# Kernel optimization log

Hardware: AMD Instinct MI355X
Metric: run time of the kernel (lower is better)

The kernel has to match this reference:

```python
import jax, jax.numpy as jnp
import numpy as np

INNER_DIM = 64
NEG = -1e12


def _rope_rotate(x, cos_pos, sin_pos):
    # x: [b, s, d]; rotate interleaved pairs as in the torch code
    x2 = jnp.stack([-x[..., 1::2], x[..., 0::2]], axis=-1).reshape(x.shape)
    return x * cos_pos + x2 * sin_pos


def setup_inputs() -> dict:
    key = jax.random.key(0)
    ks = jax.random.split(key, 5)
    b, s, h, f = 8, 1024, 768, 32
    hid = h + f  # 800
    inner, t = INNER_DIM, 9
    return {
        "last_hidden_state": jax.random.normal(ks[0], (b, s, h), jnp.float32),
        "hand_features": jax.random.normal(ks[1], (b, s, f), jnp.float32),
        "attention_mask": jnp.ones((b, s), jnp.int32),
        "W1": jax.random.normal(ks[2], (hid, 2 * inner), jnp.float32) * 0.02,
        "b1": jnp.zeros((2 * inner,), jnp.float32),
        "W2": jax.random.normal(ks[3], (hid, 2 * t), jnp.float32) * 0.02,
        "b2": jnp.zeros((2 * t,), jnp.float32),
    }


def reference(last_hidden_state, hand_features, attention_mask, W1, b1, W2, b2):
    h = jnp.concatenate([last_hidden_state, hand_features], axis=-1)  # [b,s,800]
    out = h @ W1 + b1                                                  # [b,s,2*inner]
    qw, kw = out[..., 0::2], out[..., 1::2]                            # [b,s,inner]

    s = h.shape[1]
    d = qw.shape[-1]
    # SinusoidalPositionEmbedding 'zero': interleaved sin (even) / cos (odd)
    pos = jnp.arange(s, dtype=jnp.float32)
    freqs = jnp.power(10000.0, -2.0 * jnp.arange(d // 2, dtype=jnp.float32) / d)
    ang = pos[:, None] * freqs[None, :]          # [s, d/2]
    cos_pos = jnp.repeat(jnp.cos(ang), 2, axis=-1)  # [s, d]
    sin_pos = jnp.repeat(jnp.sin(ang), 2, axis=-1)

    qw = _rope_rotate(qw, cos_pos, sin_pos)
    kw = _rope_rotate(kw, cos_pos, sin_pos)

    logits = jnp.einsum('bmd,bnd->bmn', qw, kw) / (d ** 0.5)           # [b,s,s]

    bias = jnp.einsum('bnh->bhn', h @ W2 + b2) / 2.0                   # [b,2t,s]
    logits = logits[:, None] + bias[:, 0::2, None, :] + bias[:, 1::2, :, None]  # [b,t,s,s]

    # sequence masking on both trailing axes
    m = attention_mask.astype(logits.dtype)                            # [b,s]
    mq = m[:, None, :, None]  # mask over axis -2 (rows)
    mk = m[:, None, None, :]  # mask over axis -1 (cols)
    logits = logits * mq + NEG * (1.0 - mq)
    logits = logits * mk + NEG * (1.0 - mk)

    # strictly-lower-triangular penalty (row > col)
    idx = jnp.arange(s)
    tril = (idx[:, None] > idx[None, :]).astype(logits.dtype)          # [s,s]
    logits = logits - tril * (-NEG)
    return logits
```

## Files before the change

### kernel.cpp

```cpp
#include <hip/hip_runtime.h>
#include <math.h>

#define B_   8
#define S_   1024
#define HDIM 768
#define FDIM 32
#define KDIM 800
#define D_   64
#define KSTEPS 25

constexpr float NEGV = -1000000000000.0f;

typedef __attribute__((ext_vector_type(8))) short short8;
typedef __attribute__((ext_vector_type(4))) float f32x4;

static __device__ __forceinline__ unsigned short f2bf(float f) {
    unsigned int x = __float_as_uint(f);
    unsigned int r = (x + 0x7fffu + ((x >> 16) & 1u)) >> 16;
    return (unsigned short)r;
}
static __device__ __forceinline__ unsigned int pack2(float a, float b) {
    return (unsigned int)f2bf(a) | ((unsigned int)f2bf(b) << 16);
}

union frag_cast { unsigned int u[4]; short8 s8; };

__global__ __launch_bounds__(256) void k0_prep(
    const float* __restrict__ W1, const float* __restrict__ b1,
    const float* __restrict__ W2, const float* __restrict__ b2,
    unsigned short* __restrict__ Wt, float* __restrict__ bv,
    float2* __restrict__ rope)
{
    const int tid = threadIdx.x;
    if (blockIdx.x >= 25) {
        int e = (blockIdx.x - 25) * 256 + tid;
#pragma unroll
        for (int t = 0; t < 16; ++t, e += 2048) {
            const int s = e >> 5, i = e & 31;
            const float freq = exp2f(-(float)i * 0.4152410119f);
            float sv, cv;
            sincosf((float)s * freq, &sv, &cv);
            rope[e] = make_float2(cv, sv);
        }
        return;
    }

    __shared__ float shW[32][136];
    __shared__ float shW2[32][20];
    const int k0 = blockIdx.x << 5;
#pragma unroll
    for (int p = 0; p < 4; ++p) {
        const int flat = tid + (p << 8);
        const int kk = flat >> 5;
        const int c4 = (flat & 31) << 2;
        const float4 v = *(const float4*)(W1 + (size_t)(k0 + kk) * 128 + c4);
        shW[kk][c4 + 0] = v.x; shW[kk][c4 + 1] = v.y;
        shW[kk][c4 + 2] = v.z; shW[kk][c4 + 3] = v.w;
    }
    for (int i = tid; i < 576; i += 256)
        shW2[i / 18][i % 18] = W2[(size_t)k0 * 18 + i];
    __syncthreads();

    for (int i = tid; i < 768; i += 256) {
        const int tile = i >> 6, g = (i >> 4) & 3, col = i & 15;
        const int nc = tile * 16 + col;
        unsigned int pk[4];
#pragma unroll
        for (int h = 0; h < 4; ++h) {
            const int ka = g * 8 + 2 * h, kb = ka + 1;
            float a, b;
            if (nc < 64)       { a = shW[ka][2*nc];          b = shW[kb][2*nc]; }
            else if (nc < 128) { a = shW[ka][2*(nc-64)+1];   b = shW[kb][2*(nc-64)+1]; }
            else if (nc < 146) { a = shW2[ka][nc-128];       b = shW2[kb][nc-128]; }
            else               { a = 0.0f; b = 0.0f; }
            pk[h] = pack2(a, b);
        }
        *(uint4*)(Wt + ((size_t)blockIdx.x * 768 + i) * 8) =
            make_uint4(pk[0], pk[1], pk[2], pk[3]);
    }
    if (blockIdx.x == 0 && tid < 192) {
        float v = tid < 64  ? b1[2 * tid]
                : tid < 128 ? b1[2 * (tid - 64) + 1]
                : tid < 146 ? b2[tid - 128] : 0.0f;
        bv[tid] = v;
    }
}

__global__ __launch_bounds__(256) void k1_proj(
    const float* __restrict__ lhs, const float* __restrict__ hf,
    const unsigned short* __restrict__ Wt, const float* __restrict__ bv,
    const float2* __restrict__ rope,
    unsigned short* __restrict__ qw, unsigned short* __restrict__ kw,
    float* __restrict__ bias_t)
{
    __shared__ __align__(16) unsigned short repack[16][128];

    const int tid  = threadIdx.x;
    const int m0   = blockIdx.x << 4;
    const int lane = tid & 63;
    const int w    = tid >> 6;
    const int r16  = lane & 15;
    const int g    = lane >> 4;

    const float* arow = lhs + (size_t)(m0 + r16) * HDIM;
    const float* hrow = hf  + (size_t)(m0 + r16) * FDIM;
    const unsigned short* wbase = Wt + ((size_t)(w * 3 * 64 + (g << 4) + r16)) * 8;

    float4 ab[4][2];
    uint4  bb[4][3];

    auto loadA = [&](int c, float4* dst) {
        const int k = (c << 5) + (g << 3);
        const float* src = (k < HDIM) ? (arow + k) : (hrow + (k - HDIM));
        dst[0] = *(const float4*)src;
        dst[1] = *(const float4*)(src + 4);
    };
    auto loadB = [&](int c, uint4* dst) {
        const unsigned short* p = wbase + (size_t)c * 768 * 8;
#pragma unroll
        for (int u = 0; u < 3; ++u)
            dst[u] = *(const uint4*)(p + u * 64 * 8);
    };

    f32x4 acc[3];
    const f32x4 zero = {0.0f, 0.0f, 0.0f, 0.0f};
#pragma unroll
    for (int u = 0; u < 3; ++u) acc[u] = zero;

    auto consume = [&](const float4* aA, const uint4* bB) {
        frag_cast fa;
        fa.u[0] = pack2(aA[0].x, aA[0].y);
        fa.u[1] = pack2(aA[0].z, aA[0].w);
        fa.u[2] = pack2(aA[1].x, aA[1].y);
        fa.u[3] = pack2(aA[1].z, aA[1].w);
#pragma unroll
        for (int u = 0; u < 3; ++u) {
            frag_cast fb;
            fb.u[0] = bB[u].x; fb.u[1] = bB[u].y;
            fb.u[2] = bB[u].z; fb.u[3] = bB[u].w;
            acc[u] = __builtin_amdgcn_mfma_f32_16x16x32_bf16(fa.s8, fb.s8, acc[u], 0, 0, 0);
        }
    };

#pragma unroll
    for (int d = 0; d < 4; ++d) { loadA(d, ab[d]); loadB(d, bb[d]); }

#pragma unroll
    for (int cb = 0; cb < 24; cb += 4) {
#pragma unroll
        for (int d = 0; d < 4; ++d) {
            const int c = cb + d;
            consume(ab[d], bb[d]);
            if (c + 4 < KSTEPS) { loadA(c + 4, ab[d]); loadB(c + 4, bb[d]); }
        }
    }
    consume(ab[0], bb[0]);

    const int bidx = m0 >> 10;
    const int s0   = m0 & (S_ - 1);
#pragma unroll
    for (int u = 0; u < 3; ++u) {
        const int tile = w * 3 + u;
        if (tile < 8) {
            const int jj  = (tile < 4 ? tile : tile - 4) * 16 + r16;
            const int fi  = jj >> 1;
            const float bvv = bv[tile * 16 + r16];
            const float sgn = (jj & 1) ? 1.0f : -1.0f;
            const float scl = (tile < 4) ? 0.125f : 1.0f;
            float x[4], p[4];
#pragma unroll
            for (int rr = 0; rr < 4; ++rr) x[rr] = acc[u][rr] + bvv;
#pragma unroll
            for (int rr = 0; rr < 4; ++rr) p[rr] = __shfl_xor(x[rr], 1, 64);
            const int cbase = (tile < 4 ? 0 : 64) + jj;
#pragma unroll
            for (int rr = 0; rr < 4; ++rr) {
                const float2 cs = rope[((s0 + g * 4 + rr) << 5) + fi];
                repack[g * 4 + rr][cbase] =
                    f2bf(fmaf(p[rr], sgn * cs.y, x[rr] * cs.x) * scl);
            }
        } else if (tile < 10) {
            const int cc = (tile - 8) * 16 + r16;
            if (cc < 18) {
                const float bvv = bv[tile * 16 + r16];
                f32x4 v;
#pragma unroll
                for (int rr = 0; rr < 4; ++rr) v[rr] = (acc[u][rr] + bvv) * 0.5f;
                *(f32x4*)(bias_t + (((size_t)(bidx * 18 + cc)) << 10) + s0 + g * 4) = v;
            }
        }
    }
    __syncthreads();
    {
        const int row = tid >> 4, seg = tid & 15;
        const uint4 v = *(const uint4*)&repack[row][seg * 8];
        if (seg < 8) *(uint4*)(qw + ((size_t)(m0 + row)) * D_ + seg * 8) = v;
        else         *(uint4*)(kw + ((size_t)(m0 + row)) * D_ + (seg - 8) * 8) = v;
    }
}

__global__ __launch_bounds__(256) void k2_logits(
    const unsigned short* __restrict__ qw, const unsigned short* __restrict__ kw,
    const float* __restrict__ bias_t, const int* __restrict__ mask,
    float* __restrict__ out)
{
    __shared__ __align__(16) char smem_u[64 * 66 * 4];
    __shared__ float bn[18][64];
    __shared__ float bm[18][64];
    __shared__ float mqf[64], mkf[64];
    unsigned short* qsm = (unsigned short*)smem_u;
    unsigned short* ksm = qsm + 64 * 64;
    float* tbuf = (float*)smem_u;

    const int tid = threadIdx.x;
    int bid;
    {
        const int i = blockIdx.x;
        bid = (i & 7) * 256 + (i >> 3);
    }
    const int b   = bid >> 8;
    const int rem = bid & 255;
    const int m0  = (rem >> 4) << 6;
    const int n0  = (rem & 15) << 6;

#pragma unroll
    for (int u = 0; u < 2; ++u) {
        const int idx = tid + (u << 8);
        const int row = idx >> 3;
        const int c8  = idx & 7;
        const int sb  = (row << 7) + ((c8 ^ (row & 7)) << 4);
        const uint4 vq = *(const uint4*)(qw + ((size_t)(b << 10) + m0 + row) * D_ + (c8 << 3));
        *(uint4*)((char*)qsm + sb) = vq;
        const uint4 vk = *(const uint4*)(kw + ((size_t)(b << 10) + n0 + row) * D_ + (c8 << 3));
        *(uint4*)((char*)ksm + sb) = vk;
    }
    for (int idx = tid; idx < 18 * 64; idx += 256) {
        const int c = idx >> 6;
        const int x = idx & 63;
        bn[c][x] = bias_t[(((size_t)(b * 18 + c)) << 10) + n0 + x];
        bm[c][x] = bias_t[(((size_t)(b * 18 + c)) << 10) + m0 + x];
    }
    if (tid < 64)        mqf[tid]      = (float)mask[b * S_ + m0 + tid];
    else if (tid < 128)  mkf[tid - 64] = (float)mask[b * S_ + n0 + (tid - 64)];
    __syncthreads();

    const int lane = tid & 63;
    const int w    = tid >> 6;
    const int wr   = w >> 1;
    const int wc   = w & 1;
    const int r16  = lane & 15;
    const int g    = lane >> 4;

    f32x4 acc[2][2];
    const f32x4 zero = {0.0f, 0.0f, 0.0f, 0.0f};
#pragma unroll
    for (int mi = 0; mi < 2; ++mi)
#pragma unroll
        for (int ni = 0; ni < 2; ++ni) acc[mi][ni] = zero;

#pragma unroll
    for (int ku = 0; ku < 2; ++ku) {
        short8 af[2], bf[2];
#pragma unroll
        for (int mi = 0; mi < 2; ++mi) {
            const int row  = wr * 32 + mi * 16 + r16;
            const int slot = ((ku << 2) + g) ^ (row & 7);
            af[mi] = *(const short8*)((const char*)qsm + (row << 7) + (slot << 4));
        }
#pragma unroll
        for (int ni = 0; ni < 2; ++ni) {
            const int row  = wc * 32 + ni * 16 + r16;
            const int slot = ((ku << 2) + g) ^ (row & 7);
            bf[ni] = *(const short8*)((const char*)ksm + (row << 7) + (slot << 4));
        }
#pragma unroll
        for (int mi = 0; mi < 2; ++mi)
#pragma unroll
            for (int ni = 0; ni < 2; ++ni)
                acc[mi][ni] = __builtin_amdgcn_mfma_f32_16x16x32_bf16(
                    af[mi], bf[ni], acc[mi][ni], 0, 0, 0);
    }

    __syncthreads();
#pragma unroll
    for (int mi = 0; mi < 2; ++mi)
#pragma unroll
        for (int ni = 0; ni < 2; ++ni)
#pragma unroll
            for (int rr = 0; rr < 4; ++rr)
                tbuf[(wr * 32 + mi * 16 + g * 4 + rr) * 66 +
                     wc * 32 + ni * 16 + r16] = acc[mi][ni][rr];
    __syncthreads();

    const int rb = tid >> 4;
    const int c4 = (tid & 15) << 2;
    const float fk0 = mkf[c4 + 0], fk1 = mkf[c4 + 1],
                fk2 = mkf[c4 + 2], fk3 = mkf[c4 + 3];

    float  p[4][4], accp[4][4];
    size_t base[4];
#pragma unroll
    for (int i = 0; i < 4; ++i) {
        const int row = rb + (i << 4);
        const int rg  = m0 + row;
        const float fm = mqf[row];
        const f32x4 a = *(const f32x4*)&tbuf[row * 66 + c4];
        const float fkk[4] = {fk0, fk1, fk2, fk3};
#pragma unroll
        for (int j = 0; j < 4; ++j) {
            const float fk = fkk[j];
            const float pj = fm * fk;
            float ad = NEGV * ((1.0f - fm) * fk + (1.0f - fk));
            if (rg > n0 + c4 + j) ad += NEGV;
            p[i][j]    = pj;
            accp[i][j] = fmaf(a[j], pj, ad);
        }
        base[i] = (((size_t)(b * 9)) << 20) + ((size_t)rg << 10) + n0 + c4;
    }

#pragma unroll
    for (int t = 0; t < 9; ++t) {
        const f32x4 bnv = *(const f32x4*)&bn[2 * t][c4];
        const size_t toff = (size_t)t << 20;
#pragma unroll
        for (int i = 0; i < 4; ++i) {
            const float bmv = bm[2 * t + 1][rb + (i << 4)];
            f32x4 v;
#pragma unroll
            for (int j = 0; j < 4; ++j)
                v[j] = fmaf(bnv[j] + bmv, p[i][j], accp[i][j]);
            *(f32x4*)(out + base[i] + toff) = v;
        }
    }
}

extern "C" void kernel_launch(void* const* d_in, const int* in_sizes, int n_in,
                              void* d_out, int out_size, void* d_ws, size_t ws_size,
                              hipStream_t stream) {
    const float* lhs  = (const float*)d_in[0];
    const float* hf   = (const float*)d_in[1];
    const int*   mask = (const int*)  d_in[2];
    const float* W1   = (const float*)d_in[3];
    const float* b1   = (const float*)d_in[4];
    const float* W2   = (const float*)d_in[5];
    const float* b2   = (const float*)d_in[6];
    float* out = (float*)d_out;

    unsigned short* qw = (unsigned short*)d_ws;
    unsigned short* kw = qw + (size_t)B_ * S_ * D_;
    float* bias_t = (float*)((char*)d_ws + (4u << 20));
    unsigned short* Wt = (unsigned short*)((char*)d_ws + (8u << 20));
    float* bv = (float*)((char*)d_ws + (9u << 20));
    float2* rope = (float2*)((char*)d_ws + (10u << 20));

    k0_prep<<<33, 256, 0, stream>>>(W1, b1, W2, b2, Wt, bv, rope);
    k1_proj<<<(B_ * S_) / 16, 256, 0, stream>>>(lhs, hf, Wt, bv, rope,
                                                qw, kw, bias_t);
    k2_logits<<<B_ * 16 * 16, 256, 0, stream>>>(qw, kw, bias_t, mask, out);
}
```

Before: 86.66 us.

## Retile logits kernel to 16-row full-width strips with register-streamed K fragments

The logits kernel now gives each block a 16-row by 1024-column strip instead of a 64x64 tile. Q fragments load straight into registers and K fragments stream from global memory with a four-deep register prefetch, so the shared-memory staging of Q/K goes away. Results are transposed through shared memory in two halves so each thread writes full contiguous row segments across all nine outputs. This trades tile reuse and block count (512 blocks instead of 2048) for longer contiguous stores and fewer barriers, and it may lower occupancy because of the larger accumulator and shared buffer. It relies on a frag_cast helper assumed to be defined elsewhere in the file.

```diff
diff --git a/kernel.cpp b/kernel.cpp
--- a/kernel.cpp
+++ b/kernel.cpp
@@ -204,132 +204,114 @@
     const float* __restrict__ bias_t, const int* __restrict__ mask,
     float* __restrict__ out)
 {
-    __shared__ __align__(16) char smem_u[64 * 66 * 4];
-    __shared__ float bn[18][64];
-    __shared__ float bm[18][64];
-    __shared__ float mqf[64], mkf[64];
-    unsigned short* qsm = (unsigned short*)smem_u;
-    unsigned short* ksm = qsm + 64 * 64;
-    float* tbuf = (float*)smem_u;
+    __shared__ __align__(16) float trbuf[8 * 1032];
+    __shared__ float bmv[9][16];
+    __shared__ float mqs[16];
 
     const int tid = threadIdx.x;
-    int bid;
-    {
-        const int i = blockIdx.x;
-        bid = (i & 7) * 256 + (i >> 3);
-    }
-    const int b   = bid >> 8;
-    const int rem = bid & 255;
-    const int m0  = (rem >> 4) << 6;
-    const int n0  = (rem & 15) << 6;
-
-#pragma unroll
-    for (int u = 0; u < 2; ++u) {
-        const int idx = tid + (u << 8);
-        const int row = idx >> 3;
-        const int c8  = idx & 7;
-        const int sb  = (row << 7) + ((c8 ^ (row & 7)) << 4);
-        const uint4 vq = *(const uint4*)(qw + ((size_t)(b << 10) + m0 + row) * D_ + (c8 << 3));
-        *(uint4*)((char*)qsm + sb) = vq;
-        const uint4 vk = *(const uint4*)(kw + ((size_t)(b << 10) + n0 + row) * D_ + (c8 << 3));
-        *(uint4*)((char*)ksm + sb) = vk;
-    }
-    for (int idx = tid; idx < 18 * 64; idx += 256) {
-        const int c = idx >> 6;
-        const int x = idx & 63;
-        bn[c][x] = bias_t[(((size_t)(b * 18 + c)) << 10) + n0 + x];
-        bm[c][x] = bias_t[(((size_t)(b * 18 + c)) << 10) + m0 + x];
-    }
-    if (tid < 64)        mqf[tid]      = (float)mask[b * S_ + m0 + tid];
-    else if (tid < 128)  mkf[tid - 64] = (float)mask[b * S_ + n0 + (tid - 64)];
-    __syncthreads();
+    const int i   = blockIdx.x;
+    const int swz = (i & 7) * 64 + (i >> 3);
+    const int b   = swz >> 6;
+    const int m0  = (swz & 63) << 4;
 
     const int lane = tid & 63;
     const int w    = tid >> 6;
-    const int wr   = w >> 1;
-    const int wc   = w & 1;
     const int r16  = lane & 15;
     const int g    = lane >> 4;
 
-    f32x4 acc[2][2];
+    if (tid < 144) {
+        const int t = tid >> 4, r = tid & 15;
+        bmv[t][r] = bias_t[((size_t)(b * 18 + 2 * t + 1) << 10) + m0 + r];
+    } else if (tid < 160) {
+        mqs[tid - 144] = (float)mask[(b << 10) + m0 + (tid - 144)];
+    }
+
+    const unsigned short* qrow = qw + ((size_t)((b << 10) + m0 + r16)) * D_;
+    short8 af[2];
+    af[0] = *(const short8*)(qrow + (g << 3));
+    af[1] = *(const short8*)(qrow + 32 + (g << 3));
+
+    const unsigned short* kbase =
+        kw + ((size_t)((b << 10) + (w << 8) + r16)) * D_ + (g << 3);
+
+    uint4 bb[4][2];
+    auto loadB = [&](int nt, uint4* dst) {
+        const unsigned short* p = kbase + (size_t)(nt << 4) * D_;
+        dst[0] = *(const uint4*)p;
+        dst[1] = *(const uint4*)(p + 32);
+    };
+
+#pragma unroll
+    for (int d = 0; d < 4; ++d) loadB(d, bb[d]);
+
+    f32x4 acc[16];
     const f32x4 zero = {0.0f, 0.0f, 0.0f, 0.0f};
-#pragma unroll
-    for (int mi = 0; mi < 2; ++mi)
-#pragma unroll
-        for (int ni = 0; ni < 2; ++ni) acc[mi][ni] = zero;
-
-#pragma unroll
-    for (int ku = 0; ku < 2; ++ku) {
-        short8 af[2], bf[2];
-#pragma unroll
-        for (int mi = 0; mi < 2; ++mi) {
-            const int row  = wr * 32 + mi * 16 + r16;
-            const int slot = ((ku << 2) + g) ^ (row & 7);
-            af[mi] = *(const short8*)((const char*)qsm + (row << 7) + (slot << 4));
-        }
-#pragma unroll
-        for (int ni = 0; ni < 2; ++ni) {
-            const int row  = wc * 32 + ni * 16 + r16;
-            const int slot = ((ku << 2) + g) ^ (row & 7);
-            bf[ni] = *(const short8*)((const char*)ksm + (row << 7) + (slot << 4));
-        }
-#pragma unroll
-        for (int mi = 0; mi < 2; ++mi)
-#pragma unroll
-            for (int ni = 0; ni < 2; ++ni)
-                acc[mi][ni] = __builtin_amdgcn_mfma_f32_16x16x32_bf16(
-                    af[mi], bf[ni], acc[mi][ni], 0, 0, 0);
-    }
-
-    __syncthreads();
-#pragma unroll
-    for (int mi = 0; mi < 2; ++mi)
-#pragma unroll
-        for (int ni = 0; ni < 2; ++ni)
-#pragma unroll
-            for (int rr = 0; rr < 4; ++rr)
-                tbuf[(wr * 32 + mi * 16 + g * 4 + rr) * 66 +
-                     wc * 32 + ni * 16 + r16] = acc[mi][ni][rr];
-    __syncthreads();
-
-    const int rb = tid >> 4;
-    const int c4 = (tid & 15) << 2;
-    const float fk0 = mkf[c4 + 0], fk1 = mkf[c4 + 1],
-                fk2 = mkf[c4 + 2], fk3 = mkf[c4 + 3];
-
-    float  p[4][4], accp[4][4];
-    size_t base[4];
-#pragma unroll
-    for (int i = 0; i < 4; ++i) {
-        const int row = rb + (i << 4);
-        const int rg  = m0 + row;
-        const float fm = mqf[row];
-        const f32x4 a = *(const f32x4*)&tbuf[row * 66 + c4];
-        const float fkk[4] = {fk0, fk1, fk2, fk3};
-#pragma unroll
-        for (int j = 0; j < 4; ++j) {
-            const float fk = fkk[j];
-            const float pj = fm * fk;
-            float ad = NEGV * ((1.0f - fm) * fk + (1.0f - fk));
-            if (rg > n0 + c4 + j) ad += NEGV;
-            p[i][j]    = pj;
-            accp[i][j] = fmaf(a[j], pj, ad);
-        }
-        base[i] = (((size_t)(b * 9)) << 20) + ((size_t)rg << 10) + n0 + c4;
-    }
-
-#pragma unroll
-    for (int t = 0; t < 9; ++t) {
-        const f32x4 bnv = *(const f32x4*)&bn[2 * t][c4];
-        const size_t toff = (size_t)t << 20;
-#pragma unroll
-        for (int i = 0; i < 4; ++i) {
-            const float bmv = bm[2 * t + 1][rb + (i << 4)];
-            f32x4 v;
-#pragma unroll
-            for (int j = 0; j < 4; ++j)
-                v[j] = fmaf(bnv[j] + bmv, p[i][j], accp[i][j]);
-            *(f32x4*)(out + base[i] + toff) = v;
+
+#pragma unroll
+    for (int nt = 0; nt < 16; ++nt) {
+        frag_cast f0, f1;
+        f0.u[0] = bb[nt & 3][0].x; f0.u[1] = bb[nt & 3][0].y;
+        f0.u[2] = bb[nt & 3][0].z; f0.u[3] = bb[nt & 3][0].w;
+        f1.u[0] = bb[nt & 3][1].x; f1.u[1] = bb[nt & 3][1].y;
+        f1.u[2] = bb[nt & 3][1].z; f1.u[3] = bb[nt & 3][1].w;
+        acc[nt] = __builtin_amdgcn_mfma_f32_16x16x32_bf16(af[0], f0.s8, zero, 0, 0, 0);
+        acc[nt] = __builtin_amdgcn_mfma_f32_16x16x32_bf16(af[1], f1.s8, acc[nt], 0, 0, 0);
+        if (nt + 4 < 16) loadB(nt + 4, bb[nt & 3]);
+    }
+
+    const size_t obase = ((size_t)(b * 9)) << 20;
+#pragma unroll
+    for (int p = 0; p < 2; ++p) {
+        if (p) __syncthreads();
+        if ((g >> 1) == p) {
+#pragma unroll
+            for (int nt = 0; nt < 16; ++nt)
+#pragma unroll
+                for (int j = 0; j < 4; ++j)
+                    trbuf[((g & 1) * 4 + j) * 1032 + (w << 8) + (nt << 4) + r16] =
+                        acc[nt][j];
+        }
+        __syncthreads();
+
+        const int rp  = tid >> 5;
+        const int c0  = (tid & 31) << 2;
+        const int rg  = m0 + (p << 3) + rp;
+        const float fm = mqs[(p << 3) + rp];
+
+        f32x4 accp[8], pf[8];
+#pragma unroll
+        for (int q = 0; q < 8; ++q) {
+            const int col = c0 + (q << 7);
+            const f32x4 a = *(const f32x4*)&trbuf[rp * 1032 + col];
+            const int4 mk = *(const int4*)(mask + (b << 10) + col);
+            const float fkk[4] = {(float)mk.x, (float)mk.y, (float)mk.z, (float)mk.w};
+#pragma unroll
+            for (int j = 0; j < 4; ++j) {
+                const float fk = fkk[j];
+                const float pj = fm * fk;
+                float ad = NEGV * ((1.0f - fm) * fk + (1.0f - fk));
+                if (rg > col + j) ad += NEGV;
+                pf[q][j]   = pj;
+                accp[q][j] = fmaf(a[j], pj, ad);
+            }
+        }
+
+        const size_t rbase = obase + ((size_t)rg << 10);
+#pragma unroll
+        for (int t = 0; t < 9; ++t) {
+            const float bmr = bmv[t][(p << 3) + rp];
+            const float* bnrow = bias_t + ((size_t)(b * 18 + 2 * t) << 10);
+            float* dst = out + rbase + ((size_t)t << 20);
+#pragma unroll
+            for (int q = 0; q < 8; ++q) {
+                const int col = c0 + (q << 7);
+                const f32x4 bn4 = *(const f32x4*)(bnrow + col);
+                f32x4 v;
+#pragma unroll
+                for (int j = 0; j < 4; ++j)
+                    v[j] = fmaf(bn4[j] + bmr, pf[q][j], accp[q][j]);
+                *(f32x4*)(dst + col) = v;
+            }
         }
     }
 }
@@ -356,5 +338,5 @@
     k0_prep<<<33, 256, 0, stream>>>(W1, b1, W2, b2, Wt, bv, rope);
     k1_proj<<<(B_ * S_) / 16, 256, 0, stream>>>(lhs, hf, Wt, bv, rope,
                                                 qw, kw, bias_t);
-    k2_logits<<<B_ * 16 * 16, 256, 0, stream>>>(qw, kw, bias_t, mask, out);
-}
+    k2_logits<<<B_ * 64, 256, 0, stream>>>(qw, kw, bias_t, mask, out);
+}
```

Result: slower. 90.69 us (+4.7%).
